# Kernel tuning notes

Hardware: AMD Instinct MI355X
Metric: run time of the kernel (lower is better)

## Reference

```python
import jax, jax.numpy as jnp
import numpy as np

DIM = 768
HEADS = 12
EPS = 1e-5


def setup_inputs() -> dict:
    key = jax.random.key(0)
    ks = jax.random.split(key, 12)
    B, N, C = 2, 2048, DIM
    s = 1.0 / np.sqrt(C)
    return {
        "query": jax.random.normal(ks[0], (B, N, C), jnp.float32),
        "key_in": jax.random.normal(ks[1], (B, N, C), jnp.float32),
        "value": jax.random.normal(ks[2], (B, N, C), jnp.float32),
        "Wq": jax.random.normal(ks[3], (C, C), jnp.float32) * s,
        "bq": jnp.zeros((C,), jnp.float32),
        "Wk": jax.random.normal(ks[4], (C, C), jnp.float32) * s,
        "bk": jnp.zeros((C,), jnp.float32),
        "Wv": jax.random.normal(ks[5], (C, C), jnp.float32) * s,
        "bv": jnp.zeros((C,), jnp.float32),
        "Wo": jax.random.normal(ks[6], (C, C), jnp.float32) * s,
        "bo": jnp.zeros((C,), jnp.float32),
        "gamma": jnp.ones((C,), jnp.float32),
        "beta": jnp.zeros((C,), jnp.float32),
    }


def reference(query, key_in, value, Wq, bq, Wk, bk, Wv, bv, Wo, bo, gamma, beta):
    B, N, C = query.shape
    H = HEADS
    Dh = C // H
    scale = Dh ** (-0.5)
    # projections -> [B, H, N, Dh]
    q = (query @ Wq + bq).reshape(B, N, H, Dh).transpose(0, 2, 1, 3)
    k = (key_in @ Wk + bk).reshape(B, N, H, Dh).transpose(0, 2, 1, 3)
    v = (value @ Wv + bv).reshape(B, N, H, Dh).transpose(0, 2, 1, 3)
    attn = jnp.einsum("bhnd,bhmd->bhnm", q, k) * scale
    attn = jax.nn.softmax(attn, axis=-1)  # dropout is identity in eval mode
    out = jnp.einsum("bhnm,bhmd->bhnd", attn, v)
    out = out.transpose(0, 2, 1, 3).reshape(B, N, C)
    out = out @ Wo + bo
    # residual + LayerNorm
    x = out + query
    mu = jnp.mean(x, axis=-1, keepdims=True)
    var = jnp.mean(jnp.square(x - mu), axis=-1, keepdims=True)
    return (x - mu) * jax.lax.rsqrt(var + EPS) * gamma + beta
```

## Files before the change

kernel.cpp:

```cpp
#include <hip/hip_runtime.h>
#include <hip/hip_bf16.h>


typedef unsigned short ushort_t;
typedef __bf16 bf16x8 __attribute__((ext_vector_type(8)));
typedef float  f32x4  __attribute__((ext_vector_type(4)));
typedef float  f32x16 __attribute__((ext_vector_type(16)));
typedef unsigned int uint32x4 __attribute__((ext_vector_type(4)));
typedef int    i32x2  __attribute__((ext_vector_type(2)));

constexpr int C_DIM  = 768;
constexpr int HEADS  = 12;
constexpr int DH     = 64;
constexpr int BATCH  = 2;
constexpr int SEQ    = 2048;
constexpr int MTOT   = BATCH * SEQ;
constexpr int MROWS  = BATCH * HEADS * SEQ;
constexpr int NSPLIT = 2;
constexpr int KVSPAN = SEQ / NSPLIT;
constexpr float EPS  = 1e-5f;
constexpr float SCALE = 0.125f;

constexpr size_t SZ_X = (size_t)MTOT * C_DIM;
constexpr size_t SZ_W = (size_t)C_DIM * C_DIM;
constexpr size_t B_XQ  = 0;
constexpr size_t B_XK  = B_XQ  + SZ_X * 2;
constexpr size_t B_XV  = B_XK  + SZ_X * 2;
constexpr size_t B_WQT = B_XV  + SZ_X * 2;
constexpr size_t B_WKT = B_WQT + SZ_W * 2;
constexpr size_t B_WVT = B_WKT + SZ_W * 2;
constexpr size_t B_WOT = B_WVT + SZ_W * 2;
constexpr size_t B_QH  = B_WOT + SZ_W * 2;
constexpr size_t B_KH  = B_QH  + SZ_X * 2;
constexpr size_t B_VT  = B_KH  + SZ_X * 2;
constexpr size_t B_O   = B_VT  + SZ_X * 2;
constexpr size_t B_XR  = B_O   + SZ_X * 2;
constexpr size_t B_OP  = B_XQ;
constexpr size_t B_ML  = B_OP + (size_t)NSPLIT * MROWS * DH * 2;

__device__ __forceinline__ ushort_t f2bf(float f) {
  __hip_bfloat16 h = __float2bfloat16(f);
  return __builtin_bit_cast(unsigned short, h);
}

__device__ __forceinline__ unsigned cvtpk(float lo, float hi) {
  unsigned r;
  asm("v_cvt_pk_bf16_f32 %0, %1, %2" : "=v"(r) : "v"(lo), "v"(hi));
  return r;
}
__device__ __forceinline__ float xhalf_max(float x) {
  i32x2 r = __builtin_amdgcn_permlane32_swap(
      __builtin_bit_cast(int, x), __builtin_bit_cast(int, x), false, false);
  return fmaxf(__builtin_bit_cast(float, r.x), __builtin_bit_cast(float, r.y));
}
__device__ __forceinline__ float xhalf_sum(float x) {
  i32x2 r = __builtin_amdgcn_permlane32_swap(
      __builtin_bit_cast(int, x), __builtin_bit_cast(int, x), false, false);
  return __builtin_bit_cast(float, r.x) + __builtin_bit_cast(float, r.y);
}

__device__ __forceinline__ void gload_lds16(const void* g, void* l) {
  __builtin_amdgcn_global_load_lds(
      (const __attribute__((address_space(1))) unsigned int*)g,
      (__attribute__((address_space(3))) unsigned int*)l,
      16, 0, 0);
}

__global__ __launch_bounds__(256) void cvt3_kernel(
    const float* __restrict__ s0, const float* __restrict__ s1,
    const float* __restrict__ s2,
    ushort_t* __restrict__ d0, ushort_t* __restrict__ d1,
    ushort_t* __restrict__ d2, int n4) {
  const float* src = blockIdx.y == 0 ? s0 : blockIdx.y == 1 ? s1 : s2;
  ushort_t*    dst = blockIdx.y == 0 ? d0 : blockIdx.y == 1 ? d1 : d2;
  int i = blockIdx.x * 256 + threadIdx.x;
  if (i >= n4) return;
  float4 v = ((const float4*)src)[i];
  ushort4 o;
  o.x = f2bf(v.x); o.y = f2bf(v.y); o.z = f2bf(v.z); o.w = f2bf(v.w);
  ((ushort4*)dst)[i] = o;
}

__global__ __launch_bounds__(256) void wtrans_kernel(
    const float* __restrict__ W0, const float* __restrict__ W1,
    const float* __restrict__ W2, const float* __restrict__ W3,
    ushort_t* T0, ushort_t* T1, ushort_t* T2, ushort_t* T3) {
  const float* W = blockIdx.z == 0 ? W0 : blockIdx.z == 1 ? W1 : blockIdx.z == 2 ? W2 : W3;
  ushort_t*    T = blockIdx.z == 0 ? T0 : blockIdx.z == 1 ? T1 : blockIdx.z == 2 ? T2 : T3;
  __shared__ float tile[32][33];
  int tx = threadIdx.x & 31, ty = threadIdx.x >> 5;
  int x0 = blockIdx.x * 32, y0 = blockIdx.y * 32;
#pragma unroll
  for (int i = 0; i < 32; i += 8)
    tile[ty + i][tx] = W[(size_t)(y0 + ty + i) * C_DIM + x0 + tx];
  __syncthreads();
#pragma unroll
  for (int i = 0; i < 32; i += 8)
    T[(size_t)(x0 + ty + i) * C_DIM + y0 + tx] = f2bf(tile[tx][ty + i]);
}

__device__ __forceinline__ void gemm128_mainloop(
    const ushort_t* __restrict__ A, const ushort_t* __restrict__ Bt,
    int rowBase, int colBase, ushort_t* ldsA, ushort_t* ldsB, f32x4 acc[4][4]) {
  const int tid = threadIdx.x;
  const int wave = tid >> 6, lane = tid & 63;
  const int wr = wave >> 1, wc = wave & 1;
  const int lrow = lane & 15, lk = lane >> 4;
  const int sr = tid >> 2, sk = (tid & 3) * 8;
  const int K = C_DIM;

  const ushort_t* ga0 = A  + (size_t)(rowBase + sr)      * K + sk;
  const ushort_t* ga1 = A  + (size_t)(rowBase + 64 + sr) * K + sk;
  const ushort_t* gb0 = Bt + (size_t)(colBase + sr)      * K + sk;
  const ushort_t* gb1 = Bt + (size_t)(colBase + 64 + sr) * K + sk;
  ushort_t* la = ldsA + sr * 32 + sk;
  ushort_t* lb = ldsB + sr * 32 + sk;

  for (int kt = 0; kt < K; kt += 32) {
    gload_lds16(ga0 + kt, la);
    gload_lds16(ga1 + kt, la + 64 * 32);
    gload_lds16(gb0 + kt, lb);
    gload_lds16(gb1 + kt, lb + 64 * 32);
    asm volatile("s_waitcnt vmcnt(0)" ::: "memory");
    __syncthreads();
    bf16x8 af[4], bfr[4];
#pragma unroll
    for (int m = 0; m < 4; m++)
      af[m] = *(const bf16x8*)(ldsA + (wr * 64 + m * 16 + lrow) * 32 + lk * 8);
#pragma unroll
    for (int n = 0; n < 4; n++)
      bfr[n] = *(const bf16x8*)(ldsB + (wc * 64 + n * 16 + lrow) * 32 + lk * 8);
#pragma unroll
    for (int m = 0; m < 4; m++)
#pragma unroll
      for (int n = 0; n < 4; n++)
        acc[m][n] = __builtin_amdgcn_mfma_f32_16x16x32_bf16(af[m], bfr[n], acc[m][n], 0, 0, 0);
    __syncthreads();
  }
}

__global__ __launch_bounds__(256) void gemm_qkv_kernel(
    const ushort_t* __restrict__ Xq, const ushort_t* __restrict__ Xk,
    const ushort_t* __restrict__ Xv,
    const ushort_t* __restrict__ Wqt, const ushort_t* __restrict__ Wkt,
    const ushort_t* __restrict__ Wvt,
    const float* __restrict__ bq, const float* __restrict__ bk,
    const float* __restrict__ bv,
    ushort_t* Qh, ushort_t* Kh, ushort_t* Vt) {
  const int mat = blockIdx.z;
  const ushort_t* A  = mat == 0 ? Xq  : mat == 1 ? Xk  : Xv;
  const ushort_t* Bt = mat == 0 ? Wqt : mat == 1 ? Wkt : Wvt;
  const float* bias  = mat == 0 ? bq  : mat == 1 ? bk  : bv;

  __shared__ __align__(16) ushort_t ldsA[128 * 32];
  __shared__ __align__(16) ushort_t ldsB[128 * 32];

  const int rowBase = blockIdx.y * 128;
  const int colBase = blockIdx.x * 128;
  f32x4 acc[4][4];
#pragma unroll
  for (int m = 0; m < 4; m++)
#pragma unroll
    for (int n = 0; n < 4; n++)
#pragma unroll
      for (int r = 0; r < 4; r++) acc[m][n][r] = 0.f;

  gemm128_mainloop(A, Bt, rowBase, colBase, ldsA, ldsB, acc);

  const int lane = threadIdx.x & 63, wave = threadIdx.x >> 6;
  const int wr = wave >> 1, wc = wave & 1;
  const int lrow = lane & 15, lk = lane >> 4;
  const float sc = (mat == 0) ? SCALE : 1.0f;

  __hip_bfloat16* dqk = (__hip_bfloat16*)(mat == 0 ? Qh : Kh);
  __hip_bfloat16* dvt = (__hip_bfloat16*)Vt;
#pragma unroll
  for (int n = 0; n < 4; n++) {
    const int col = colBase + wc * 64 + n * 16 + lrow;
    const float bval = bias[col];
    const int hh = col >> 6, dd = col & 63;
#pragma unroll
    for (int m = 0; m < 4; m++) {
#pragma unroll
      for (int r = 0; r < 4; r++) {
        const int row = rowBase + wr * 64 + m * 16 + lk * 4 + r;
        const int bb = row >> 11, nn = row & 2047;
        const float val = (acc[m][n][r] + bval) * sc;
        if (mat < 2) {
          dqk[(((size_t)(bb * HEADS + hh) * SEQ + nn) << 6) + dd] = __float2bfloat16(val);
        } else {
          dvt[((size_t)(bb * HEADS + hh) * DH + dd) * SEQ + nn] = __float2bfloat16(val);
        }
      }
    }
  }
}

__global__ __launch_bounds__(256) void attn_kernel(
    const ushort_t* __restrict__ Qh, const ushort_t* __restrict__ Kh,
    const ushort_t* __restrict__ Vt, ushort_t* __restrict__ Opart,
    float2* __restrict__ Ml) {
  const int fb   = blockIdx.x;
  const int xcd  = fb & 7;
  const int slot = fb >> 3;
  const int g    = slot >> 5;
  const int rem  = slot & 31;
  const int qt    = rem & 15;
  const int split = rem >> 4;
  const int bh    = xcd + 8 * g;

  const ushort_t* Qp = Qh + (size_t)bh * SEQ * DH;
  const ushort_t* Kp = Kh + (size_t)bh * SEQ * DH;
  const ushort_t* Vp = Vt + (size_t)bh * DH * SEQ;

  const int tid = threadIdx.x, wave = tid >> 6, lane = tid & 63;
  const int lq = lane & 31;
  const int hi = lane >> 5;
  const int qrow0 = qt * 128 + wave * 32;
  const int kv0 = split * KVSPAN;

  bf16x8 qf[4];
#pragma unroll
  for (int ks = 0; ks < 4; ks++)
    qf[ks] = *(const bf16x8*)&Qp[(size_t)(qrow0 + lq) * DH + ks * 16 + hi * 8];

  bf16x8 kfA[4], kfB[4];
#pragma unroll
  for (int ks = 0; ks < 4; ks++)
    kfA[ks] = *(const bf16x8*)&Kp[(size_t)(kv0 + lq) * DH + ks * 16 + hi * 8];

  f32x16 oacc[2];
#pragma unroll
  for (int dt = 0; dt < 2; dt++)
#pragma unroll
    for (int r = 0; r < 16; r++) oacc[dt][r] = 0.f;
  float mrun = -3e38f, lrun = 0.f;

#pragma unroll 1
  for (int it = 0; it < KVSPAN / 32; it++) {
    const int kv = kv0 + it * 32;
    const bf16x8* kc = (it & 1) ? kfB : kfA;
    bf16x8*       kn = (it & 1) ? kfA : kfB;

    f32x16 st;
#pragma unroll
    for (int r = 0; r < 16; r++) st[r] = 0.f;
    __builtin_amdgcn_s_setprio(1);
#pragma unroll
    for (int ks = 0; ks < 4; ks++)
      st = __builtin_amdgcn_mfma_f32_32x32x16_bf16(kc[ks], qf[ks], st, 0, 0, 0);
    __builtin_amdgcn_s_setprio(0);

    bf16x8 vf[2][2];
#pragma unroll
    for (int dt = 0; dt < 2; dt++)
#pragma unroll
      for (int s = 0; s < 2; s++)
        vf[dt][s] = *(const bf16x8*)&Vp[(size_t)(dt * 32 + lq) * SEQ + kv + s * 16 + hi * 8];

    const int nkv = kv0 + (((it + 1) & (KVSPAN / 32 - 1)) * 32);
#pragma unroll
    for (int ks = 0; ks < 4; ks++)
      kn[ks] = *(const bf16x8*)&Kp[(size_t)(nkv + lq) * DH + ks * 16 + hi * 8];

    float tm = st[0];
#pragma unroll
    for (int r = 1; r < 16; r++) tm = fmaxf(tm, st[r]);
    tm = xhalf_max(tm);
    float m = mrun;
    if (!__all(tm <= mrun + 8.f)) {
      m = fmaxf(mrun, tm);
      const float fac = __expf(mrun - m);
      mrun = m;
      lrun *= fac;
#pragma unroll
      for (int dt = 0; dt < 2; dt++)
#pragma unroll
        for (int r = 0; r < 16; r++) oacc[dt][r] *= fac;
    }
    float ps = 0.f;
#pragma unroll
    for (int r = 0; r < 16; r++) {
      float p = __expf(st[r] - m);
      st[r] = p;
      ps += p;
    }
    lrun += xhalf_sum(ps);

    unsigned pk[8];
#pragma unroll
    for (int i = 0; i < 8; i++) pk[i] = cvtpk(st[2 * i], st[2 * i + 1]);
    uint32x4 a0, a1;
    {
      i32x2 r02 = __builtin_amdgcn_permlane32_swap((int)pk[0], (int)pk[2], false, false);
      i32x2 r13 = __builtin_amdgcn_permlane32_swap((int)pk[1], (int)pk[3], false, false);
      a0.x = (unsigned)r02.x; a0.y = (unsigned)r13.x;
      a0.z = (unsigned)r02.y; a0.w = (unsigned)r13.y;
      i32x2 r46 = __builtin_amdgcn_permlane32_swap((int)pk[4], (int)pk[6], false, false);
      i32x2 r57 = __builtin_amdgcn_permlane32_swap((int)pk[5], (int)pk[7], false, false);
      a1.x = (unsigned)r46.x; a1.y = (unsigned)r57.x;
      a1.z = (unsigned)r46.y; a1.w = (unsigned)r57.y;
    }
    const bf16x8 w0 = __builtin_bit_cast(bf16x8, a0);
    const bf16x8 w1 = __builtin_bit_cast(bf16x8, a1);

    __builtin_amdgcn_s_setprio(1);
#pragma unroll
    for (int dt = 0; dt < 2; dt++) {
      oacc[dt] = __builtin_amdgcn_mfma_f32_32x32x16_bf16(vf[dt][0], w0, oacc[dt], 0, 0, 0);
      oacc[dt] = __builtin_amdgcn_mfma_f32_32x32x16_bf16(vf[dt][1], w1, oacc[dt], 0, 0, 0);
    }
    __builtin_amdgcn_s_setprio(0);
  }

  const int rid = bh * SEQ + qrow0 + lq;
  ushort_t* Oprow = Opart + ((size_t)split * MROWS + rid) * DH;
#pragma unroll
  for (int dt = 0; dt < 2; dt++)
#pragma unroll
    for (int gg = 0; gg < 4; gg++) {
      ushort4 w;
      w.x = f2bf(oacc[dt][gg * 4 + 0]);
      w.y = f2bf(oacc[dt][gg * 4 + 1]);
      w.z = f2bf(oacc[dt][gg * 4 + 2]);
      w.w = f2bf(oacc[dt][gg * 4 + 3]);
      *(ushort4*)&Oprow[dt * 32 + gg * 8 + hi * 4] = w;
    }
  if (hi == 0) Ml[(size_t)split * MROWS + rid] = make_float2(mrun, lrun);
}

__global__ __launch_bounds__(256) void attn_combine_kernel(
    const ushort_t* __restrict__ Opart, const float2* __restrict__ Ml,
    ushort_t* __restrict__ O) {
  const int t = threadIdx.x;
  const int rid = blockIdx.x * 4 + (t >> 6);
  const int col = t & 63;
  const float2 ml0 = Ml[rid];
  const float2 ml1 = Ml[(size_t)MROWS + rid];
  const float M = fmaxf(ml0.x, ml1.x);
  const float w0 = __expf(ml0.x - M), w1 = __expf(ml1.x - M);
  const float inv = 1.f / (w0 * ml0.y + w1 * ml1.y);
  const float o0 = __bfloat162float(__builtin_bit_cast(__hip_bfloat16,
                     Opart[(size_t)rid * DH + col]));
  const float o1 = __bfloat162float(__builtin_bit_cast(__hip_bfloat16,
                     Opart[((size_t)MROWS + rid) * DH + col]));
  const float o = (w0 * o0 + w1 * o1) * inv;
  const int bh = rid >> 11, n = rid & 2047;
  const int b = bh / HEADS, h = bh - b * HEADS;
  ((__hip_bfloat16*)O)[(size_t)(b * SEQ + n) * C_DIM + h * DH + col] =
      __float2bfloat16(o);
}

__global__ __launch_bounds__(256) void gemm_out_kernel(
    const ushort_t* __restrict__ Obf, const ushort_t* __restrict__ Wot,
    const float* __restrict__ bo, const float* __restrict__ query,
    float* __restrict__ X) {
  __shared__ __align__(16) ushort_t ldsA[128 * 32];
  __shared__ __align__(16) ushort_t ldsB[128 * 32];
  const int rowBase = blockIdx.y * 128;
  const int colBase = blockIdx.x * 128;
  f32x4 acc[4][4];
#pragma unroll
  for (int m = 0; m < 4; m++)
#pragma unroll
    for (int n = 0; n < 4; n++)
#pragma unroll
      for (int r = 0; r < 4; r++) acc[m][n][r] = 0.f;

  gemm128_mainloop(Obf, Wot, rowBase, colBase, ldsA, ldsB, acc);

  const int lane = threadIdx.x & 63, wave = threadIdx.x >> 6;
  const int wr = wave >> 1, wc = wave & 1;
  const int lrow = lane & 15, lk = lane >> 4;
#pragma unroll
  for (int n = 0; n < 4; n++) {
    const int col = colBase + wc * 64 + n * 16 + lrow;
    const float bval = bo[col];
#pragma unroll
    for (int m = 0; m < 4; m++) {
#pragma unroll
      for (int r = 0; r < 4; r++) {
        const int row = rowBase + wr * 64 + m * 16 + lk * 4 + r;
        const size_t idx = (size_t)row * C_DIM + col;
        X[idx] = acc[m][n][r] + bval + query[idx];
      }
    }
  }
}

__global__ __launch_bounds__(256) void ln_kernel(
    const float* __restrict__ X, const float* __restrict__ gamma,
    const float* __restrict__ beta, float* __restrict__ out) {
  const int row = blockIdx.x, tid = threadIdx.x;
  const float* xr = X + (size_t)row * C_DIM;
  float x0 = xr[tid], x1 = xr[tid + 256], x2 = xr[tid + 512];
  float s = x0 + x1 + x2;
  float sq = x0 * x0 + x1 * x1 + x2 * x2;
#pragma unroll
  for (int off = 32; off; off >>= 1) {
    s  += __shfl_xor(s, off);
    sq += __shfl_xor(sq, off);
  }
  __shared__ float as_[4], aq_[4];
  if ((tid & 63) == 0) { as_[tid >> 6] = s; aq_[tid >> 6] = sq; }
  __syncthreads();
  s  = as_[0] + as_[1] + as_[2] + as_[3];
  sq = aq_[0] + aq_[1] + aq_[2] + aq_[3];
  const float mean = s * (1.f / C_DIM);
  const float var  = sq * (1.f / C_DIM) - mean * mean;
  const float rstd = rsqrtf(var + EPS);
  float* orow = out + (size_t)row * C_DIM;
  orow[tid]       = (x0 - mean) * rstd * gamma[tid]       + beta[tid];
  orow[tid + 256] = (x1 - mean) * rstd * gamma[tid + 256] + beta[tid + 256];
  orow[tid + 512] = (x2 - mean) * rstd * gamma[tid + 512] + beta[tid + 512];
}

extern "C" void kernel_launch(void* const* d_in, const int* in_sizes, int n_in,
                              void* d_out, int out_size, void* d_ws, size_t ws_size,
                              hipStream_t stream) {
  (void)in_sizes; (void)n_in; (void)out_size; (void)ws_size;
  const float* query  = (const float*)d_in[0];
  const float* key_in = (const float*)d_in[1];
  const float* value  = (const float*)d_in[2];
  const float* Wq = (const float*)d_in[3];
  const float* bq = (const float*)d_in[4];
  const float* Wk = (const float*)d_in[5];
  const float* bk = (const float*)d_in[6];
  const float* Wv = (const float*)d_in[7];
  const float* bv = (const float*)d_in[8];
  const float* Wo = (const float*)d_in[9];
  const float* bo = (const float*)d_in[10];
  const float* gamma = (const float*)d_in[11];
  const float* beta  = (const float*)d_in[12];

  char* ws = (char*)d_ws;
  ushort_t* Xq  = (ushort_t*)(ws + B_XQ);
  ushort_t* Xk  = (ushort_t*)(ws + B_XK);
  ushort_t* Xv  = (ushort_t*)(ws + B_XV);
  ushort_t* Wqt = (ushort_t*)(ws + B_WQT);
  ushort_t* Wkt = (ushort_t*)(ws + B_WKT);
  ushort_t* Wvt = (ushort_t*)(ws + B_WVT);
  ushort_t* Wot = (ushort_t*)(ws + B_WOT);
  ushort_t* Qh  = (ushort_t*)(ws + B_QH);
  ushort_t* Kh  = (ushort_t*)(ws + B_KH);
  ushort_t* Vt  = (ushort_t*)(ws + B_VT);
  ushort_t* Obf = (ushort_t*)(ws + B_O);
  float*    Xr  = (float*)(ws + B_XR);
  ushort_t* Opart = (ushort_t*)(ws + B_OP);
  float2*   Ml    = (float2*)(ws + B_ML);
  float*    out = (float*)d_out;

  const int n4 = (int)(SZ_X / 4);
  cvt3_kernel<<<dim3(n4 / 256, 3), 256, 0, stream>>>(query, key_in, value,
                                                     Xq, Xk, Xv, n4);

  wtrans_kernel<<<dim3(24, 24, 4), 256, 0, stream>>>(Wq, Wk, Wv, Wo, Wqt, Wkt, Wvt, Wot);

  gemm_qkv_kernel<<<dim3(6, 32, 3), 256, 0, stream>>>(Xq, Xk, Xv, Wqt, Wkt, Wvt,
                                                      bq, bk, bv, Qh, Kh, Vt);

  attn_kernel<<<8 * 3 * 16 * NSPLIT, 256, 0, stream>>>(Qh, Kh, Vt, Opart, Ml);

  attn_combine_kernel<<<MROWS / 4, 256, 0, stream>>>(Opart, Ml, Obf);

  gemm_out_kernel<<<dim3(6, 32), 256, 0, stream>>>(Obf, Wot, bo, query, Xr);

  ln_kernel<<<MTOT, 256, 0, stream>>>(Xr, gamma, beta, out);
}
```

Measured before the change: 277.7 us.

## Store Q/K/V in MFMA-fragment-native layout for coalesced attention loads

The QKV projection epilogue now writes Q, K and V into a fragment-tiled layout, so each lane's 8-element bf16x8 operand for the 32x32x16 MFMA sits contiguously at lane*8 inside a 512-element block. The attention kernel then loads Q, K and V fragments as fully contiguous 1 KB wavefront reads instead of strided row reads, with V no longer needing a transposed [D][SEQ] layout. This is meant to cut global/L2 traffic inefficiency in the attention inner loop. In exchange the GEMM epilogue's scattered 2-byte stores get more complex address arithmetic and may coalesce differently.

```diff
diff --git a/kernel.cpp b/kernel.cpp
--- a/kernel.cpp
+++ b/kernel.cpp
@@ -18,6 +18,7 @@
 constexpr int MROWS  = BATCH * HEADS * SEQ;
 constexpr int NSPLIT = 2;
 constexpr int KVSPAN = SEQ / NSPLIT;
+constexpr int HSZ    = SEQ * DH;
 constexpr float EPS  = 1e-5f;
 constexpr float SCALE = 0.125f;
 
@@ -146,7 +147,7 @@
     const ushort_t* __restrict__ Wvt,
     const float* __restrict__ bq, const float* __restrict__ bk,
     const float* __restrict__ bv,
-    ushort_t* Qh, ushort_t* Kh, ushort_t* Vt) {
+    ushort_t* QF, ushort_t* KF, ushort_t* VF) {
   const int mat = blockIdx.z;
   const ushort_t* A  = mat == 0 ? Xq  : mat == 1 ? Xk  : Xv;
   const ushort_t* Bt = mat == 0 ? Wqt : mat == 1 ? Wkt : Wvt;
@@ -172,8 +173,8 @@
   const int lrow = lane & 15, lk = lane >> 4;
   const float sc = (mat == 0) ? SCALE : 1.0f;
 
-  __hip_bfloat16* dqk = (__hip_bfloat16*)(mat == 0 ? Qh : Kh);
-  __hip_bfloat16* dvt = (__hip_bfloat16*)Vt;
+  __hip_bfloat16* dqk = (__hip_bfloat16*)(mat == 0 ? QF : KF);
+  __hip_bfloat16* dvt = (__hip_bfloat16*)VF;
 #pragma unroll
   for (int n = 0; n < 4; n++) {
     const int col = colBase + wc * 64 + n * 16 + lrow;
@@ -185,11 +186,21 @@
       for (int r = 0; r < 4; r++) {
         const int row = rowBase + wr * 64 + m * 16 + lk * 4 + r;
         const int bb = row >> 11, nn = row & 2047;
+        const int bh = bb * HEADS + hh;
         const float val = (acc[m][n][r] + bval) * sc;
         if (mat < 2) {
-          dqk[(((size_t)(bb * HEADS + hh) * SEQ + nn) << 6) + dd] = __float2bfloat16(val);
+          const int t32 = nn >> 5, r32 = nn & 31;
+          const int ks = dd >> 4, hi2 = (dd >> 3) & 1, j = dd & 7;
+          const size_t addr = (size_t)bh * HSZ + (size_t)(((t32 << 2) + ks) << 9)
+                              + ((r32 + (hi2 << 5)) << 3) + j;
+          dqk[addr] = __float2bfloat16(val);
         } else {
-          dvt[((size_t)(bb * HEADS + hh) * DH + dd) * SEQ + nn] = __float2bfloat16(val);
+          const int kvt = nn >> 5, s = (nn >> 4) & 1, hi2 = (nn >> 3) & 1, j = nn & 7;
+          const int dt = dd >> 5, r32 = dd & 31;
+          const size_t addr = (size_t)bh * HSZ
+                              + (size_t)((((kvt << 1) + dt) * 2 + s) << 9)
+                              + ((r32 + (hi2 << 5)) << 3) + j;
+          dvt[addr] = __float2bfloat16(val);
         }
       }
     }
@@ -197,8 +208,8 @@
 }
 
 __global__ __launch_bounds__(256) void attn_kernel(
-    const ushort_t* __restrict__ Qh, const ushort_t* __restrict__ Kh,
-    const ushort_t* __restrict__ Vt, ushort_t* __restrict__ Opart,
+    const ushort_t* __restrict__ QF, const ushort_t* __restrict__ KF,
+    const ushort_t* __restrict__ VF, ushort_t* __restrict__ Opart,
     float2* __restrict__ Ml) {
   const int fb   = blockIdx.x;
   const int xcd  = fb & 7;
@@ -209,25 +220,26 @@
   const int split = rem >> 4;
   const int bh    = xcd + 8 * g;
 
-  const ushort_t* Qp = Qh + (size_t)bh * SEQ * DH;
-  const ushort_t* Kp = Kh + (size_t)bh * SEQ * DH;
-  const ushort_t* Vp = Vt + (size_t)bh * DH * SEQ;
-
   const int tid = threadIdx.x, wave = tid >> 6, lane = tid & 63;
   const int lq = lane & 31;
   const int hi = lane >> 5;
   const int qrow0 = qt * 128 + wave * 32;
-  const int kv0 = split * KVSPAN;
+  const int qt32 = qrow0 >> 5;
+  const int kvt0 = split * (KVSPAN / 32);
+
+  const ushort_t* Qb = QF + (size_t)bh * HSZ + (lane << 3);
+  const ushort_t* Kb = KF + (size_t)bh * HSZ + (lane << 3);
+  const ushort_t* Vb = VF + (size_t)bh * HSZ + (lane << 3);
 
   bf16x8 qf[4];
 #pragma unroll
   for (int ks = 0; ks < 4; ks++)
-    qf[ks] = *(const bf16x8*)&Qp[(size_t)(qrow0 + lq) * DH + ks * 16 + hi * 8];
+    qf[ks] = *(const bf16x8*)(Qb + (((qt32 << 2) + ks) << 9));
 
   bf16x8 kfA[4], kfB[4];
 #pragma unroll
   for (int ks = 0; ks < 4; ks++)
-    kfA[ks] = *(const bf16x8*)&Kp[(size_t)(kv0 + lq) * DH + ks * 16 + hi * 8];
+    kfA[ks] = *(const bf16x8*)(Kb + (((kvt0 << 2) + ks) << 9));
 
   f32x16 oacc[2];
 #pragma unroll
@@ -238,7 +250,7 @@
 
 #pragma unroll 1
   for (int it = 0; it < KVSPAN / 32; it++) {
-    const int kv = kv0 + it * 32;
+    const int kvt = kvt0 + it;
     const bf16x8* kc = (it & 1) ? kfB : kfA;
     bf16x8*       kn = (it & 1) ? kfA : kfB;
 
@@ -256,12 +268,12 @@
     for (int dt = 0; dt < 2; dt++)
 #pragma unroll
       for (int s = 0; s < 2; s++)
-        vf[dt][s] = *(const bf16x8*)&Vp[(size_t)(dt * 32 + lq) * SEQ + kv + s * 16 + hi * 8];
-
-    const int nkv = kv0 + (((it + 1) & (KVSPAN / 32 - 1)) * 32);
+        vf[dt][s] = *(const bf16x8*)(Vb + (((((kvt << 1) + dt) << 1) + s) << 9));
+
+    const int nkvt = kvt0 + ((it + 1) & (KVSPAN / 32 - 1));
 #pragma unroll
     for (int ks = 0; ks < 4; ks++)
-      kn[ks] = *(const bf16x8*)&Kp[(size_t)(nkv + lq) * DH + ks * 16 + hi * 8];
+      kn[ks] = *(const bf16x8*)(Kb + (((nkvt << 2) + ks) << 9));
 
     float tm = st[0];
 #pragma unroll
@@ -441,9 +453,9 @@
   ushort_t* Wkt = (ushort_t*)(ws + B_WKT);
   ushort_t* Wvt = (ushort_t*)(ws + B_WVT);
   ushort_t* Wot = (ushort_t*)(ws + B_WOT);
-  ushort_t* Qh  = (ushort_t*)(ws + B_QH);
-  ushort_t* Kh  = (ushort_t*)(ws + B_KH);
-  ushort_t* Vt  = (ushort_t*)(ws + B_VT);
+  ushort_t* QF  = (ushort_t*)(ws + B_QH);
+  ushort_t* KF  = (ushort_t*)(ws + B_KH);
+  ushort_t* VF  = (ushort_t*)(ws + B_VT);
   ushort_t* Obf = (ushort_t*)(ws + B_O);
   float*    Xr  = (float*)(ws + B_XR);
   ushort_t* Opart = (ushort_t*)(ws + B_OP);
@@ -457,9 +469,9 @@
   wtrans_kernel<<<dim3(24, 24, 4), 256, 0, stream>>>(Wq, Wk, Wv, Wo, Wqt, Wkt, Wvt, Wot);
 
   gemm_qkv_kernel<<<dim3(6, 32, 3), 256, 0, stream>>>(Xq, Xk, Xv, Wqt, Wkt, Wvt,
-                                                      bq, bk, bv, Qh, Kh, Vt);
-
-  attn_kernel<<<8 * 3 * 16 * NSPLIT, 256, 0, stream>>>(Qh, Kh, Vt, Opart, Ml);
+                                                      bq, bk, bv, QF, KF, VF);
+
+  attn_kernel<<<8 * 3 * 16 * NSPLIT, 256, 0, stream>>>(QF, KF, VF, Opart, Ml);
 
   attn_combine_kernel<<<MROWS / 4, 256, 0, stream>>>(Opart, Ml, Obf);
 
```

Measured after the change: 249.5 us. 10.2% less time.
